# Performance work log

Measured on AMD Instinct MI355X. Metric: run time of the kernel, lower is better.

## Reference

```python
import jax, jax.numpy as jnp
import numpy as np

B, F, D = 16384, 26, 128

def setup_inputs() -> dict:
    key = jax.random.key(0)
    k1, k2 = jax.random.split(key)
    dense_features = jax.random.normal(k1, (B, D), dtype=jnp.float32)
    sparse_values = jax.random.normal(k2, (B, F, D), dtype=jnp.float32)
    return {"dense_features": dense_features, "sparse_values": sparse_values}

def reference(dense_features, sparse_values):
    # sparse-dense dots: [B, F]
    sd = jnp.einsum('bfd,bd->bf', sparse_values, dense_features)
    # pairwise sparse-sparse dots: [B, F, F]
    ss = jnp.einsum('bfd,bgd->bfg', sparse_values, sparse_values)
    # upper triangle (i<j) in row-major order matches itertools.combinations
    iu, ju = jnp.triu_indices(F, k=1)
    pairs = ss[:, iu, ju]  # [B, F*(F-1)/2]
    # concat: dense (B,D) + sparse-dense (B,F) + pairwise (B, C(F,2))
    return jnp.concatenate([dense_features, sd, pairs], axis=1)
```

## Files before the change

### kernel.cpp

```cpp
#include <hip/hip_runtime.h>
#include <hip/hip_bf16.h>

#define NBATCH 16384
#define NF 26
#define ND 128
#define BPB 4
#define OUTW 479

typedef __attribute__((ext_vector_type(8))) __bf16 bf16x8;
typedef __attribute__((ext_vector_type(4))) float floatx4;

__device__ __forceinline__ bf16x8 cvt8(float4 a, float4 b) {
    return (bf16x8){(__bf16)a.x, (__bf16)a.y, (__bf16)a.z, (__bf16)a.w,
                    (__bf16)b.x, (__bf16)b.y, (__bf16)b.z, (__bf16)b.w};
}

__global__ __launch_bounds__(256, 4)
void interaction_kernel(const float* __restrict__ dense,
                        const float* __restrict__ sparse,
                        float* __restrict__ out)
{
    __shared__ __align__(16) float stage[BPB * OUTW];

    const int t    = threadIdx.x;
    const int blk  = blockIdx.x;
    const int b0   = blk * BPB;
    const int wave = t >> 6;
    const int lane = t & 63;
    const int quad = lane >> 4;
    const int lrow = lane & 15;

    if (t < BPB * 32) {
        int batch = t >> 5, chunk = t & 31;
        *(float4*)&stage[batch * OUTW + chunk * 4] =
            *(const float4*)&dense[(size_t)(b0 + batch) * ND + chunk * 4];
    }

    const int batch = b0 + wave;
    const float* base0 = (lrow == 0)
        ? dense  + (size_t)batch * ND
        : sparse + ((size_t)batch * NF + (lrow - 1)) * ND;
    int r1 = 15 + lrow; if (r1 > NF - 1) r1 = NF - 1;
    const float* base1 = sparse + ((size_t)batch * NF + r1) * ND;

    bf16x8 f0[4], f1[4];
    #pragma unroll
    for (int k = 0; k < 4; ++k) {
        const int off = k * 32 + quad * 8;
        float4 a0 = *(const float4*)(base0 + off);
        float4 a1 = *(const float4*)(base0 + off + 4);
        float4 c0 = *(const float4*)(base1 + off);
        float4 c1 = *(const float4*)(base1 + off + 4);
        f0[k] = cvt8(a0, a1);
        f1[k] = cvt8(c0, c1);
    }

    floatx4 c00 = {0.f, 0.f, 0.f, 0.f};
    floatx4 c01 = {0.f, 0.f, 0.f, 0.f};
    floatx4 c11 = {0.f, 0.f, 0.f, 0.f};
    #pragma unroll
    for (int k = 0; k < 4; ++k) {
        c00 = __builtin_amdgcn_mfma_f32_16x16x32_bf16(f0[k], f0[k], c00, 0, 0, 0);
        c01 = __builtin_amdgcn_mfma_f32_16x16x32_bf16(f0[k], f1[k], c01, 0, 0, 0);
        c11 = __builtin_amdgcn_mfma_f32_16x16x32_bf16(f1[k], f1[k], c11, 0, 0, 0);
    }

    {
        float* sb = &stage[wave * OUTW];
        auto scatter = [&](int r, int c, float v) {
            if (c <= NF && r < c) {
                int idx = (r == 0)
                    ? (ND - 1 + c)
                    : (ND + NF + (((r - 1) * (52 - r)) >> 1) + c - r - 1);
                sb[idx] = v;
            }
        };
        #pragma unroll
        for (int rr = 0; rr < 4; ++rr) {
            int r = quad * 4 + rr;
            scatter(r,      lrow,      c00[rr]);
            scatter(r,      16 + lrow, c01[rr]);
            scatter(16 + r, 16 + lrow, c11[rr]);
        }
    }
    __syncthreads();

    const size_t outbase = (size_t)blk * (BPB * OUTW);
    for (int c = t; c < (BPB * OUTW) / 4; c += 256) {
        *(uint4*)&out[outbase + c * 4] = *(const uint4*)&stage[c * 4];
    }
}

extern "C" void kernel_launch(void* const* d_in, const int* in_sizes, int n_in,
                              void* d_out, int out_size, void* d_ws, size_t ws_size,
                              hipStream_t stream) {
    const float* dense  = (const float*)d_in[0];
    const float* sparse = (const float*)d_in[1];
    float* out = (float*)d_out;
    dim3 grid(NBATCH / BPB);
    dim3 block(256);
    hipLaunchKernelGGL(interaction_kernel, grid, block, 0, stream, dense, sparse, out);
}
```

Baseline: 309.6 us.

## Process two batches per wave with per-wave LDS staging and no block barrier

Each wave now handles two batch rows in a loop instead of one, and the grid shrinks to match. The block-wide __syncthreads and the shared 4-batch staging buffer are replaced by a per-wave 352-float LDS buffer for only the interaction outputs, synchronized with a wave barrier plus an LDS waitcnt. The dense features are written straight from registers to global memory, and the interaction results are copied out with scalar per-lane stores. This removes block-level synchronization and staging of the dense part, at the cost of unaligned scalar stores in place of 16-byte vector stores.

```diff
diff --git a/kernel.cpp b/kernel.cpp
--- a/kernel.cpp
+++ b/kernel.cpp
@@ -4,13 +4,15 @@
 #define NBATCH 16384
 #define NF 26
 #define ND 128
-#define BPB 4
 #define OUTW 479
+#define WPB 4
+#define GPW 2
+#define NBLK (NBATCH / (WPB * GPW))
 
 typedef __attribute__((ext_vector_type(8))) __bf16 bf16x8;
 typedef __attribute__((ext_vector_type(4))) float floatx4;
 
-__device__ __forceinline__ bf16x8 cvt8(float4 a, float4 b) {
+__device__ __forceinline__ bf16x8 cvt8(floatx4 a, floatx4 b) {
     return (bf16x8){(__bf16)a.x, (__bf16)a.y, (__bf16)a.z, (__bf16)a.w,
                     (__bf16)b.x, (__bf16)b.y, (__bf16)b.z, (__bf16)b.w};
 }
@@ -20,58 +22,60 @@
                         const float* __restrict__ sparse,
                         float* __restrict__ out)
 {
-    __shared__ __align__(16) float stage[BPB * OUTW];
+    __shared__ float stage[WPB * 352];
 
     const int t    = threadIdx.x;
-    const int blk  = blockIdx.x;
-    const int b0   = blk * BPB;
     const int wave = t >> 6;
     const int lane = t & 63;
     const int quad = lane >> 4;
     const int lrow = lane & 15;
 
-    if (t < BPB * 32) {
-        int batch = t >> 5, chunk = t & 31;
-        *(float4*)&stage[batch * OUTW + chunk * 4] =
-            *(const float4*)&dense[(size_t)(b0 + batch) * ND + chunk * 4];
-    }
+    float* sb = &stage[wave * 352];
 
-    const int batch = b0 + wave;
-    const float* base0 = (lrow == 0)
-        ? dense  + (size_t)batch * ND
-        : sparse + ((size_t)batch * NF + (lrow - 1)) * ND;
     int r1 = 15 + lrow; if (r1 > NF - 1) r1 = NF - 1;
-    const float* base1 = sparse + ((size_t)batch * NF + r1) * ND;
 
-    bf16x8 f0[4], f1[4];
-    #pragma unroll
-    for (int k = 0; k < 4; ++k) {
-        const int off = k * 32 + quad * 8;
-        float4 a0 = *(const float4*)(base0 + off);
-        float4 a1 = *(const float4*)(base0 + off + 4);
-        float4 c0 = *(const float4*)(base1 + off);
-        float4 c1 = *(const float4*)(base1 + off + 4);
-        f0[k] = cvt8(a0, a1);
-        f1[k] = cvt8(c0, c1);
-    }
+    for (int g = 0; g < GPW; ++g) {
+        const int b = (blockIdx.x * WPB + wave) * GPW + g;
+        float* outrow = out + (size_t)b * OUTW;
 
-    floatx4 c00 = {0.f, 0.f, 0.f, 0.f};
-    floatx4 c01 = {0.f, 0.f, 0.f, 0.f};
-    floatx4 c11 = {0.f, 0.f, 0.f, 0.f};
-    #pragma unroll
-    for (int k = 0; k < 4; ++k) {
-        c00 = __builtin_amdgcn_mfma_f32_16x16x32_bf16(f0[k], f0[k], c00, 0, 0, 0);
-        c01 = __builtin_amdgcn_mfma_f32_16x16x32_bf16(f0[k], f1[k], c01, 0, 0, 0);
-        c11 = __builtin_amdgcn_mfma_f32_16x16x32_bf16(f1[k], f1[k], c11, 0, 0, 0);
-    }
+        float d0 = dense[(size_t)b * ND + lane];
+        float d1 = dense[(size_t)b * ND + 64 + lane];
 
-    {
-        float* sb = &stage[wave * OUTW];
+        const float* base0 = (lrow == 0)
+            ? dense  + (size_t)b * ND
+            : sparse + ((size_t)b * NF + (lrow - 1)) * ND;
+        const float* base1 = sparse + ((size_t)b * NF + r1) * ND;
+
+        bf16x8 f0[4], f1[4];
+        #pragma unroll
+        for (int k = 0; k < 4; ++k) {
+            const int off = k * 32 + quad * 8;
+            floatx4 a0 = *(const floatx4*)(base0 + off);
+            floatx4 a1 = *(const floatx4*)(base0 + off + 4);
+            floatx4 c0 = *(const floatx4*)(base1 + off);
+            floatx4 c1 = *(const floatx4*)(base1 + off + 4);
+            f0[k] = cvt8(a0, a1);
+            f1[k] = cvt8(c0, c1);
+        }
+
+        floatx4 c00 = {0.f, 0.f, 0.f, 0.f};
+        floatx4 c01 = {0.f, 0.f, 0.f, 0.f};
+        floatx4 c11 = {0.f, 0.f, 0.f, 0.f};
+        #pragma unroll
+        for (int k = 0; k < 4; ++k) {
+            c00 = __builtin_amdgcn_mfma_f32_16x16x32_bf16(f0[k], f0[k], c00, 0, 0, 0);
+            c01 = __builtin_amdgcn_mfma_f32_16x16x32_bf16(f0[k], f1[k], c01, 0, 0, 0);
+            c11 = __builtin_amdgcn_mfma_f32_16x16x32_bf16(f1[k], f1[k], c11, 0, 0, 0);
+        }
+
+        outrow[lane]      = d0;
+        outrow[64 + lane] = d1;
+
         auto scatter = [&](int r, int c, float v) {
             if (c <= NF && r < c) {
                 int idx = (r == 0)
-                    ? (ND - 1 + c)
-                    : (ND + NF + (((r - 1) * (52 - r)) >> 1) + c - r - 1);
+                    ? (c - 1)
+                    : (NF + (((r - 1) * (52 - r)) >> 1) + c - r - 1);
                 sb[idx] = v;
             }
         };
@@ -82,12 +86,16 @@
             scatter(r,      16 + lrow, c01[rr]);
             scatter(16 + r, 16 + lrow, c11[rr]);
         }
-    }
-    __syncthreads();
 
-    const size_t outbase = (size_t)blk * (BPB * OUTW);
-    for (int c = t; c < (BPB * OUTW) / 4; c += 256) {
-        *(uint4*)&out[outbase + c * 4] = *(const uint4*)&stage[c * 4];
+        __builtin_amdgcn_wave_barrier();
+        __builtin_amdgcn_s_waitcnt(0xc07f);
+        __builtin_amdgcn_wave_barrier();
+
+        #pragma unroll
+        for (int j = 0; j < 6; ++j) {
+            int idx = j * 64 + lane;
+            if (idx < 351) outrow[128 + idx] = sb[idx];
+        }
     }
 }
 
@@ -97,7 +105,7 @@
     const float* dense  = (const float*)d_in[0];
     const float* sparse = (const float*)d_in[1];
     float* out = (float*)d_out;
-    dim3 grid(NBATCH / BPB);
+    dim3 grid(NBLK);
     dim3 block(256);
     hipLaunchKernelGGL(interaction_kernel, grid, block, 0, stream, dense, sparse, out);
 }
```

Measured after the change: 311.0 us. No clear change (+0.4%).
